# Optimization experiments

Hardware: AMD Instinct MI355X
Metric: run time of the kernel (lower is better)

The kernel has to match this reference:

```python
import jax, jax.numpy as jnp
import numpy as np

B, N, C, H, W = 4, 8, 256, 64, 64
SCALE = 2
D = C * SCALE  # embed_dim*scale, head_size with n_heads=1
EPS = 1e-6


def setup_inputs() -> dict:
    key = jax.random.key(0)
    ks = jax.random.split(key, 6)
    sc = lambda k, sh, f: jax.random.normal(k, sh, jnp.float32) * f
    return {
        "q": jax.random.normal(ks[0], (B, C), jnp.float32),
        "c": jax.random.normal(ks[1], (B, N, C, H, W), jnp.float32),
        "g": jnp.ones((C,), jnp.float32),                 # RMSNorm weight
        "Wq": sc(ks[2], (D, C), C ** -0.5),               # proj_q weight
        "Wkv": sc(ks[3], (2 * D, C), C ** -0.5),          # proj_kv weight
        "Wo": sc(ks[4], (C, D), D ** -0.5),               # proj_out weight
        "bo": jnp.zeros((C,), jnp.float32),               # proj_out bias
    }


def reference(q, c, g, Wq, Wkv, Wo, bo):
    # c: [B,N,C,H,W] -> [B,H,W,N,C]
    cp = jnp.transpose(c, (0, 3, 4, 1, 2))
    # RMSNorm over channel dim
    cn = cp * jax.lax.rsqrt(jnp.mean(cp * cp, axis=-1, keepdims=True) + EPS) * g
    # per-pixel, per-token k/v projection: [B,H,W,N,2D]
    kv = jnp.einsum('bhwnc,dc->bhwnd', cn, Wkv)
    k, v = jnp.split(kv, 2, axis=-1)                      # each [B,H,W,N,D]
    qp = q @ Wq.T                                         # [B,D]
    # broadcast single query over spatial grid; softmax over N context tokens
    dots = jnp.einsum('bd,bhwnd->bhwn', qp, k) * (D ** -0.5)
    att = jax.nn.softmax(dots, axis=-1)                   # [B,H,W,N]
    hvec = jnp.einsum('bhwn,bhwnd->bhwd', att, v)         # [B,H,W,D]
    out = hvec @ Wo.T + bo                                # [B,H,W,C]
    return jnp.transpose(out, (0, 3, 1, 2))               # [B,C,H,W]
```

## Files before the change

kernel.cpp:

```cpp
#include <hip/hip_runtime.h>


typedef __attribute__((ext_vector_type(8))) short short8;
typedef __attribute__((ext_vector_type(4))) float floatx4;

static __device__ __forceinline__ short f2bf(float f) {
  unsigned u = __float_as_uint(f);
  u += 0x7fffu + ((u >> 16) & 1u);
  return (short)(u >> 16);
}

__global__ __launch_bounds__(256) void pre_kernel(
    const float* __restrict__ q, const float* __restrict__ g,
    const float* __restrict__ Wq, const float* __restrict__ Wkv,
    const float* __restrict__ Wo, unsigned char* __restrict__ ws) {
  short* WovgB = (short*)ws;
  float* gqk = (float*)(ws + 131072);
  const int blk = blockIdx.x, tid = threadIdx.x;
  if (blk < 64) {
    const int c = tid, i0 = blk * 4;
    float s0 = 0.f, s1 = 0.f, s2 = 0.f, s3 = 0.f;
    #pragma unroll 8
    for (int d = 0; d < 512; ++d) {
      const float wv = Wkv[(512 + d) * 256 + c];
      s0 = fmaf(Wo[(i0 + 0) * 512 + d], wv, s0);
      s1 = fmaf(Wo[(i0 + 1) * 512 + d], wv, s1);
      s2 = fmaf(Wo[(i0 + 2) * 512 + d], wv, s2);
      s3 = fmaf(Wo[(i0 + 3) * 512 + d], wv, s3);
    }
    const float gc = g[c];
    const float sv[4] = {s0, s1, s2, s3};
    const int sg = c >> 5, q2 = (c >> 3) & 3, jj = c & 7;
    #pragma unroll
    for (int r = 0; r < 4; ++r) {
      const int i = i0 + r;
      const int it = i >> 4, m = i & 15;
      WovgB[((((it * 8 + sg) * 4 + q2) * 16) + m) * 8 + jj] = f2bf(sv[r] * gc);
    }
  } else {
    const int b = blk - 64;
    __shared__ float qps[512];
    for (int d = tid; d < 512; d += 256) {
      float s = 0.f;
      #pragma unroll 16
      for (int cc = 0; cc < 256; ++cc)
        s = fmaf(Wq[d * 256 + cc], q[b * 256 + cc], s);
      qps[d] = s;
    }
    __syncthreads();
    const int c = tid;
    float s = 0.f;
    #pragma unroll 16
    for (int d = 0; d < 512; ++d)
      s = fmaf(Wkv[d * 256 + c], qps[d], s);
    gqk[b * 256 + c] = s * g[c] * 0.044194173824159216f;
  }
}

__global__ __launch_bounds__(512) void attn_kernel(
    const float* __restrict__ cin, const float* __restrict__ bo,
    const unsigned char* __restrict__ ws, float* __restrict__ out) {
  const short8* Av = (const short8*)ws;
  const float* gqk = (const float*)(ws + 131072);
  const int blk = blockIdx.x;
  const int b = blk >> 7, h = (blk >> 1) & 63, hf = blk & 1;
  const int tid = threadIdx.x;
  const int lane = tid & 63, w = tid >> 6;
  const int px = lane & 31, cgh = lane >> 5;
  const int cg = w * 2 + cgh;

  __shared__ short tB[8][2][64][8];
  __shared__ float redS[2][8][32], redD[2][8][32];

  float rg[16];
  #pragma unroll
  for (int j = 0; j < 16; ++j) rg[j] = gqk[b * 256 + cg * 16 + j];

  float t_reg[16];
  #pragma unroll
  for (int j = 0; j < 16; ++j) t_reg[j] = 0.f;
  float mM = -1e30f, zZ = 0.f;

  const float* cb = cin + ((size_t)(b * 8) * 256 + cg * 16) * 4096
                        + h * 64 + hf * 32 + px;
  float vcur[16], vnxt[16];
  #pragma unroll
  for (int j = 0; j < 16; ++j) vcur[j] = cb[(size_t)j * 4096];

  #pragma unroll
  for (int n = 0; n < 8; ++n) {
    float ssq = 0.f, dt = 0.f;
    #pragma unroll
    for (int j = 0; j < 16; ++j) {
      ssq = fmaf(vcur[j], vcur[j], ssq);
      dt = fmaf(vcur[j], rg[j], dt);
    }
    ssq += __shfl_xor(ssq, 32);
    dt  += __shfl_xor(dt, 32);
    if (cgh == 0) { redS[n & 1][w][px] = ssq; redD[n & 1][w][px] = dt; }
    if (n < 7) {
      const float* cp = cb + (size_t)(n + 1) * 1048576;
      #pragma unroll
      for (int j = 0; j < 16; ++j) vnxt[j] = cp[(size_t)j * 4096];
    }
    __syncthreads();
    float S = 0.f, Dt = 0.f;
    #pragma unroll
    for (int ww = 0; ww < 8; ++ww) { S += redS[n & 1][ww][px]; Dt += redD[n & 1][ww][px]; }
    const float invr = rsqrtf(S * (1.f / 256.f) + 1e-6f);
    const float d = Dt * invr;
    const float mn = fmaxf(mM, d);
    const float al = __expf(mM - mn);
    const float e = __expf(d - mn);
    zZ = zZ * al + e;
    mM = mn;
    const float wn = e * invr;
    #pragma unroll
    for (int j = 0; j < 16; ++j) t_reg[j] = fmaf(wn, vcur[j], t_reg[j] * al);
    #pragma unroll
    for (int j = 0; j < 16; ++j) vcur[j] = vnxt[j];
  }

  {
    const float invZ = 1.f / zZ;
    const int nt = px >> 4, mm = px & 15;
    const int s = cg >> 1;
    #pragma unroll
    for (int h2 = 0; h2 < 2; ++h2) {
      const int q = (cg & 1) * 2 + h2;
      short8 pk;
      #pragma unroll
      for (int jj = 0; jj < 8; ++jj) pk[jj] = f2bf(t_reg[h2 * 8 + jj] * invZ);
      *(short8*)(&tB[s][nt][q * 16 + mm][0]) = pk;
    }
  }
  __syncthreads();

  const int q = lane >> 4, m = lane & 15;
  const short8* Bv = (const short8*)tB;
  floatx4 acc[2][2];
  #pragma unroll
  for (int mt = 0; mt < 2; ++mt)
    #pragma unroll
    for (int nt = 0; nt < 2; ++nt) acc[mt][nt] = (floatx4){0.f, 0.f, 0.f, 0.f};
  #pragma unroll
  for (int s = 0; s < 8; ++s) {
    short8 a[2];
    #pragma unroll
    for (int mt = 0; mt < 2; ++mt)
      a[mt] = Av[(((w * 2 + mt) * 8 + s) * 4 + q) * 16 + m];
    #pragma unroll
    for (int nt = 0; nt < 2; ++nt) {
      const short8 bf = Bv[(s * 2 + nt) * 64 + lane];
      #pragma unroll
      for (int mt = 0; mt < 2; ++mt)
        acc[mt][nt] = __builtin_amdgcn_mfma_f32_16x16x32_bf16(a[mt], bf, acc[mt][nt], 0, 0, 0);
    }
  }
  float* ob = out + (size_t)b * 256 * 4096 + h * 64 + hf * 32;
  #pragma unroll
  for (int mt = 0; mt < 2; ++mt) {
    float bov[4];
    #pragma unroll
    for (int r = 0; r < 4; ++r) bov[r] = bo[w * 32 + mt * 16 + q * 4 + r];
    #pragma unroll
    for (int nt = 0; nt < 2; ++nt)
      #pragma unroll
      for (int r = 0; r < 4; ++r) {
        const int i = w * 32 + mt * 16 + q * 4 + r;
        ob[(size_t)i * 4096 + nt * 16 + m] = acc[mt][nt][r] + bov[r];
      }
  }
}

extern "C" void kernel_launch(void* const* d_in, const int* in_sizes, int n_in,
                              void* d_out, int out_size, void* d_ws, size_t ws_size,
                              hipStream_t stream) {
  const float* q   = (const float*)d_in[0];
  const float* c   = (const float*)d_in[1];
  const float* g   = (const float*)d_in[2];
  const float* Wq  = (const float*)d_in[3];
  const float* Wkv = (const float*)d_in[4];
  const float* Wo  = (const float*)d_in[5];
  const float* bo  = (const float*)d_in[6];
  float* out = (float*)d_out;
  unsigned char* ws = (unsigned char*)d_ws;
  pre_kernel<<<68, 256, 0, stream>>>(q, g, Wq, Wkv, Wo, ws);
  attn_kernel<<<512, 512, 0, stream>>>(c, bo, ws, out);
}
```

Baseline: 255.1 us.

## Split attention blocks to 16-pixel tiles with 256 threads and interleaved channels

The attention kernel now launches 1024 blocks of 256 threads, each covering 16 pixels instead of 32, with channels interleaved across lane subgroups. Block indices are swizzled so that consecutive blocks map to different rows. The channel reduction uses two shuffles plus a 4-wave shared sum, and each wave's MFMA output loop covers four output tiles against one B tile. The aim is more blocks for load balancing and finer-grained concurrency, at the cost of 64-byte rather than 128-byte contiguous global segments per row.

```diff
diff --git a/kernel.cpp b/kernel.cpp
--- a/kernel.cpp
+++ b/kernel.cpp
@@ -57,35 +57,36 @@
   }
 }
 
-__global__ __launch_bounds__(512) void attn_kernel(
+__global__ __launch_bounds__(256) void attn_kernel(
     const float* __restrict__ cin, const float* __restrict__ bo,
     const unsigned char* __restrict__ ws, float* __restrict__ out) {
   const short8* Av = (const short8*)ws;
   const float* gqk = (const float*)(ws + 131072);
-  const int blk = blockIdx.x;
-  const int b = blk >> 7, h = (blk >> 1) & 63, hf = blk & 1;
+  const int u = blockIdx.x;
+  const int bh = ((u >> 5) << 3) | (u & 7);
+  const int qg = (u >> 3) & 3;
+  const int b = bh >> 6, h = bh & 63;
   const int tid = threadIdx.x;
   const int lane = tid & 63, w = tid >> 6;
-  const int px = lane & 31, cgh = lane >> 5;
-  const int cg = w * 2 + cgh;
+  const int sub = lane >> 4, pxl = lane & 15;
 
-  __shared__ short tB[8][2][64][8];
-  __shared__ float redS[2][8][32], redD[2][8][32];
+  __shared__ short tB[8][64][8];
+  __shared__ float redS[2][4][16], redD[2][4][16];
 
   float rg[16];
   #pragma unroll
-  for (int j = 0; j < 16; ++j) rg[j] = gqk[b * 256 + cg * 16 + j];
+  for (int j = 0; j < 16; ++j) rg[j] = gqk[b * 256 + w * 64 + j * 4 + sub];
 
   float t_reg[16];
   #pragma unroll
   for (int j = 0; j < 16; ++j) t_reg[j] = 0.f;
   float mM = -1e30f, zZ = 0.f;
 
-  const float* cb = cin + ((size_t)(b * 8) * 256 + cg * 16) * 4096
-                        + h * 64 + hf * 32 + px;
+  const float* cb = cin + ((size_t)(b * 8) * 256 + w * 64 + sub) * 4096
+                        + h * 64 + qg * 16 + pxl;
   float vcur[16], vnxt[16];
   #pragma unroll
-  for (int j = 0; j < 16; ++j) vcur[j] = cb[(size_t)j * 4096];
+  for (int j = 0; j < 16; ++j) vcur[j] = cb[(size_t)j * 16384];
 
   #pragma unroll
   for (int n = 0; n < 8; ++n) {
@@ -95,18 +96,18 @@
       ssq = fmaf(vcur[j], vcur[j], ssq);
       dt = fmaf(vcur[j], rg[j], dt);
     }
-    ssq += __shfl_xor(ssq, 32);
-    dt  += __shfl_xor(dt, 32);
-    if (cgh == 0) { redS[n & 1][w][px] = ssq; redD[n & 1][w][px] = dt; }
+    ssq += __shfl_xor(ssq, 16); ssq += __shfl_xor(ssq, 32);
+    dt  += __shfl_xor(dt, 16);  dt  += __shfl_xor(dt, 32);
+    if (sub == 0) { redS[n & 1][w][pxl] = ssq; redD[n & 1][w][pxl] = dt; }
     if (n < 7) {
       const float* cp = cb + (size_t)(n + 1) * 1048576;
       #pragma unroll
-      for (int j = 0; j < 16; ++j) vnxt[j] = cp[(size_t)j * 4096];
+      for (int j = 0; j < 16; ++j) vnxt[j] = cp[(size_t)j * 16384];
     }
     __syncthreads();
     float S = 0.f, Dt = 0.f;
     #pragma unroll
-    for (int ww = 0; ww < 8; ++ww) { S += redS[n & 1][ww][px]; Dt += redD[n & 1][ww][px]; }
+    for (int ww = 0; ww < 4; ++ww) { S += redS[n & 1][ww][pxl]; Dt += redD[n & 1][ww][pxl]; }
     const float invr = rsqrtf(S * (1.f / 256.f) + 1e-6f);
     const float d = Dt * invr;
     const float mn = fmaxf(mM, d);
@@ -123,53 +124,40 @@
 
   {
     const float invZ = 1.f / zZ;
-    const int nt = px >> 4, mm = px & 15;
-    const int s = cg >> 1;
     #pragma unroll
-    for (int h2 = 0; h2 < 2; ++h2) {
-      const int q = (cg & 1) * 2 + h2;
-      short8 pk;
-      #pragma unroll
-      for (int jj = 0; jj < 8; ++jj) pk[jj] = f2bf(t_reg[h2 * 8 + jj] * invZ);
-      *(short8*)(&tB[s][nt][q * 16 + mm][0]) = pk;
+    for (int j = 0; j < 16; ++j) {
+      const int k_in = (j & 7) * 4 + sub;
+      tB[w * 2 + (j >> 3)][(k_in >> 3) * 16 + pxl][k_in & 7] =
+          f2bf(t_reg[j] * invZ);
     }
   }
   __syncthreads();
 
   const int q = lane >> 4, m = lane & 15;
   const short8* Bv = (const short8*)tB;
-  floatx4 acc[2][2];
+  floatx4 acc[4];
   #pragma unroll
-  for (int mt = 0; mt < 2; ++mt)
-    #pragma unroll
-    for (int nt = 0; nt < 2; ++nt) acc[mt][nt] = (floatx4){0.f, 0.f, 0.f, 0.f};
+  for (int it4 = 0; it4 < 4; ++it4) acc[it4] = (floatx4){0.f, 0.f, 0.f, 0.f};
   #pragma unroll
   for (int s = 0; s < 8; ++s) {
-    short8 a[2];
+    const short8 bf = Bv[s * 64 + lane];
     #pragma unroll
-    for (int mt = 0; mt < 2; ++mt)
-      a[mt] = Av[(((w * 2 + mt) * 8 + s) * 4 + q) * 16 + m];
-    #pragma unroll
-    for (int nt = 0; nt < 2; ++nt) {
-      const short8 bf = Bv[(s * 2 + nt) * 64 + lane];
-      #pragma unroll
-      for (int mt = 0; mt < 2; ++mt)
-        acc[mt][nt] = __builtin_amdgcn_mfma_f32_16x16x32_bf16(a[mt], bf, acc[mt][nt], 0, 0, 0);
+    for (int it4 = 0; it4 < 4; ++it4) {
+      const short8 a = Av[(((w * 4 + it4) * 8 + s) * 4 + q) * 16 + m];
+      acc[it4] = __builtin_amdgcn_mfma_f32_16x16x32_bf16(a, bf, acc[it4], 0, 0, 0);
     }
   }
-  float* ob = out + (size_t)b * 256 * 4096 + h * 64 + hf * 32;
+  float* ob = out + (size_t)b * 1048576 + h * 64 + qg * 16;
   #pragma unroll
-  for (int mt = 0; mt < 2; ++mt) {
+  for (int it4 = 0; it4 < 4; ++it4) {
     float bov[4];
     #pragma unroll
-    for (int r = 0; r < 4; ++r) bov[r] = bo[w * 32 + mt * 16 + q * 4 + r];
+    for (int r = 0; r < 4; ++r) bov[r] = bo[(w * 4 + it4) * 16 + q * 4 + r];
     #pragma unroll
-    for (int nt = 0; nt < 2; ++nt)
-      #pragma unroll
-      for (int r = 0; r < 4; ++r) {
-        const int i = w * 32 + mt * 16 + q * 4 + r;
-        ob[(size_t)i * 4096 + nt * 16 + m] = acc[mt][nt][r] + bov[r];
-      }
+    for (int r = 0; r < 4; ++r) {
+      const int i = (w * 4 + it4) * 16 + q * 4 + r;
+      ob[(size_t)i * 4096 + m] = acc[it4][r] + bov[r];
+    }
   }
 }
 
@@ -186,5 +174,5 @@
   float* out = (float*)d_out;
   unsigned char* ws = (unsigned char*)d_ws;
   pre_kernel<<<68, 256, 0, stream>>>(q, g, Wq, Wkv, Wo, ws);
-  attn_kernel<<<512, 512, 0, stream>>>(c, bo, ws, out);
+  attn_kernel<<<1024, 256, 0, stream>>>(c, bo, ws, out);
 }
```

Result: no change. 255.6 us (+0.2%).

## Load all context tokens upfront and replace online softmax with single-pass reductions

Applied to the files above, without the earlier changes.

All 8 context tokens' 16-channel slices are loaded into registers (128 floats per thread) before any computation, so every global load is in flight at once instead of double-buffering one token ahead. The per-token syncthreads is replaced by a single barrier, with partial sums stored in per-token shared-memory slots. The online softmax becomes an explicit max, exp and sum pass followed by one weighted accumulation. This raises register pressure heavily at 512 threads per block, which may reduce occupancy or cause spills.

```diff
diff --git a/kernel.cpp b/kernel.cpp
--- a/kernel.cpp
+++ b/kernel.cpp
@@ -70,59 +70,67 @@
   const int cg = w * 2 + cgh;
 
   __shared__ short tB[8][2][64][8];
-  __shared__ float redS[2][8][32], redD[2][8][32];
+  __shared__ float redS[8][8][32], redD[8][8][32];
 
   float rg[16];
   #pragma unroll
   for (int j = 0; j < 16; ++j) rg[j] = gqk[b * 256 + cg * 16 + j];
 
-  float t_reg[16];
-  #pragma unroll
-  for (int j = 0; j < 16; ++j) t_reg[j] = 0.f;
-  float mM = -1e30f, zZ = 0.f;
-
   const float* cb = cin + ((size_t)(b * 8) * 256 + cg * 16) * 4096
                         + h * 64 + hf * 32 + px;
-  float vcur[16], vnxt[16];
+  float vals[8][16];
   #pragma unroll
-  for (int j = 0; j < 16; ++j) vcur[j] = cb[(size_t)j * 4096];
+  for (int n = 0; n < 8; ++n) {
+    const float* cp = cb + (size_t)n * 1048576;
+    #pragma unroll
+    for (int j = 0; j < 16; ++j) vals[n][j] = cp[(size_t)j * 4096];
+  }
 
   #pragma unroll
   for (int n = 0; n < 8; ++n) {
     float ssq = 0.f, dt = 0.f;
     #pragma unroll
     for (int j = 0; j < 16; ++j) {
-      ssq = fmaf(vcur[j], vcur[j], ssq);
-      dt = fmaf(vcur[j], rg[j], dt);
+      ssq = fmaf(vals[n][j], vals[n][j], ssq);
+      dt = fmaf(vals[n][j], rg[j], dt);
     }
     ssq += __shfl_xor(ssq, 32);
     dt  += __shfl_xor(dt, 32);
-    if (cgh == 0) { redS[n & 1][w][px] = ssq; redD[n & 1][w][px] = dt; }
-    if (n < 7) {
-      const float* cp = cb + (size_t)(n + 1) * 1048576;
-      #pragma unroll
-      for (int j = 0; j < 16; ++j) vnxt[j] = cp[(size_t)j * 4096];
-    }
-    __syncthreads();
+    if (cgh == 0) { redS[n][w][px] = ssq; redD[n][w][px] = dt; }
+  }
+  __syncthreads();
+
+  float dots[8], ivr[8];
+  float mx = -1e30f;
+  #pragma unroll
+  for (int n = 0; n < 8; ++n) {
     float S = 0.f, Dt = 0.f;
     #pragma unroll
-    for (int ww = 0; ww < 8; ++ww) { S += redS[n & 1][ww][px]; Dt += redD[n & 1][ww][px]; }
-    const float invr = rsqrtf(S * (1.f / 256.f) + 1e-6f);
-    const float d = Dt * invr;
-    const float mn = fmaxf(mM, d);
-    const float al = __expf(mM - mn);
-    const float e = __expf(d - mn);
-    zZ = zZ * al + e;
-    mM = mn;
-    const float wn = e * invr;
+    for (int ww = 0; ww < 8; ++ww) { S += redS[n][ww][px]; Dt += redD[n][ww][px]; }
+    ivr[n] = rsqrtf(S * (1.f / 256.f) + 1e-6f);
+    dots[n] = Dt * ivr[n];
+    mx = fmaxf(mx, dots[n]);
+  }
+  float Z = 0.f;
+  float wn[8];
+  #pragma unroll
+  for (int n = 0; n < 8; ++n) {
+    const float e = __expf(dots[n] - mx);
+    Z += e;
+    wn[n] = e * ivr[n];
+  }
+  const float invZ = 1.f / Z;
+
+  float t_reg[16];
+  #pragma unroll
+  for (int j = 0; j < 16; ++j) {
+    float a = 0.f;
     #pragma unroll
-    for (int j = 0; j < 16; ++j) t_reg[j] = fmaf(wn, vcur[j], t_reg[j] * al);
-    #pragma unroll
-    for (int j = 0; j < 16; ++j) vcur[j] = vnxt[j];
+    for (int n = 0; n < 8; ++n) a = fmaf(wn[n], vals[n][j], a);
+    t_reg[j] = a * invZ;
   }
 
   {
-    const float invZ = 1.f / zZ;
     const int nt = px >> 4, mm = px & 15;
     const int s = cg >> 1;
     #pragma unroll
@@ -130,7 +138,7 @@
       const int q = (cg & 1) * 2 + h2;
       short8 pk;
       #pragma unroll
-      for (int jj = 0; jj < 8; ++jj) pk[jj] = f2bf(t_reg[h2 * 8 + jj] * invZ);
+      for (int jj = 0; jj < 8; ++jj) pk[jj] = f2bf(t_reg[h2 * 8 + jj]);
       *(short8*)(&tB[s][nt][q * 16 + mm][0]) = pk;
     }
   }
@@ -157,7 +165,7 @@
         acc[mt][nt] = __builtin_amdgcn_mfma_f32_16x16x32_bf16(a[mt], bf, acc[mt][nt], 0, 0, 0);
     }
   }
-  float* ob = out + (size_t)b * 256 * 4096 + h * 64 + hf * 32;
+  float* ob = out + (size_t)b * 1048576 + h * 64 + hf * 32;
   #pragma unroll
   for (int mt = 0; mt < 2; ++mt) {
     float bov[4];
```

After: 256.3 us. About the same (+0.5%).
